# Performance work log

Measured on AMD Instinct MI355X. Metric: run time of the kernel, lower is better.

## Reference

```python
import jax, jax.numpy as jnp
import numpy as np
import math

HIDDEN = 4096
N_HEADS = 32
HEAD_DIM = HIDDEN // N_HEADS
ADAPTER_LEN = 10
BATCH = 1
SEQ = 2048
ROPE_BASE = 10000.0


def setup_inputs() -> dict:
    key = jax.random.key(0)
    ks = jax.random.split(key, 8)
    hidden_states = jax.random.normal(ks[0], (BATCH, SEQ, HIDDEN), dtype=jnp.float32)
    # additive causal mask [B,1,q,kv] with 0 on allowed, large negative on masked
    neg = jnp.finfo(jnp.float32).min
    causal = jnp.triu(jnp.full((SEQ, SEQ), neg, dtype=jnp.float32), k=1)
    attention_mask = jnp.broadcast_to(causal, (BATCH, 1, SEQ, SEQ))
    position_ids = jnp.broadcast_to(jnp.arange(SEQ, dtype=jnp.int64 if jax.config.read('jax_enable_x64') else jnp.int32)[None, :], (BATCH, SEQ))
    s = 0.02
    Wq = jax.random.normal(ks[1], (HIDDEN, HIDDEN), dtype=jnp.float32) * s
    Wk = jax.random.normal(ks[2], (HIDDEN, HIDDEN), dtype=jnp.float32) * s
    Wv = jax.random.normal(ks[3], (HIDDEN, HIDDEN), dtype=jnp.float32) * s
    Wo = jax.random.normal(ks[4], (HIDDEN, HIDDEN), dtype=jnp.float32) * s
    adapter_prefix = jax.random.normal(ks[5], (ADAPTER_LEN, HIDDEN), dtype=jnp.float32) * s
    gate = jnp.zeros((N_HEADS, 1, 1), dtype=jnp.float32) + 0.1  # nonzero so gated path is exercised
    return {"hidden_states": hidden_states, "attention_mask": attention_mask,
            "position_ids": position_ids, "Wq": Wq, "Wk": Wk, "Wv": Wv, "Wo": Wo,
            "adapter_prefix": adapter_prefix, "gate": gate}


def _rotate_half(x):
    x1, x2 = jnp.split(x, 2, axis=-1)
    return jnp.concatenate([-x2, x1], axis=-1)


def _rope_cos_sin(position_ids, head_dim, dtype):
    # inv_freq: [hd/2]
    inv_freq = 1.0 / (ROPE_BASE ** (jnp.arange(0, head_dim, 2, dtype=jnp.float32) / head_dim))
    freqs = position_ids.astype(jnp.float32)[:, :, None] * inv_freq[None, None, :]  # [B,S,hd/2]
    emb = jnp.concatenate([freqs, freqs], axis=-1)  # [B,S,hd]
    cos = jnp.cos(emb)[:, None, :, :].astype(dtype)  # [B,1,S,hd]
    sin = jnp.sin(emb)[:, None, :, :].astype(dtype)
    return cos, sin


def reference(hidden_states, attention_mask, position_ids, Wq, Wk, Wv, Wo, adapter_prefix, gate):
    B, S, H = hidden_states.shape
    nh, hd = N_HEADS, HEAD_DIM
    plen = adapter_prefix.shape[0]

    def proj(x, W):  # torch Linear: x @ W.T
        return jnp.einsum('...h,oh->...o', x, W)

    q = proj(hidden_states, Wq).reshape(B, S, nh, hd).transpose(0, 2, 1, 3)  # [B,nh,S,hd]
    k = proj(hidden_states, Wk).reshape(B, S, nh, hd).transpose(0, 2, 1, 3)
    v = proj(hidden_states, Wv).reshape(B, S, nh, hd).transpose(0, 2, 1, 3)

    cos, sin = _rope_cos_sin(position_ids, hd, q.dtype)
    q = q * cos + _rotate_half(q) * sin
    k = k * cos + _rotate_half(k) * sin

    # adapter prefix KV (bsz must be 1 per original view semantics; no RoPE applied)
    kp = proj(adapter_prefix, Wk).reshape(B, plen, nh, hd).transpose(0, 2, 1, 3)  # [B,nh,plen,hd]
    vp = proj(adapter_prefix, Wv).reshape(B, plen, nh, hd).transpose(0, 2, 1, 3)
    K = jnp.concatenate([kp, k], axis=2)  # [B,nh,plen+S,hd]
    V = jnp.concatenate([vp, v], axis=2)

    mask = jnp.concatenate([jnp.zeros((B, 1, S, plen), dtype=attention_mask.dtype), attention_mask], axis=-1)
    scores = jnp.einsum('bhqd,bhkd->bhqk', q, K) / math.sqrt(hd)
    scores = scores + mask
    scores = jnp.maximum(scores, jnp.finfo(scores.dtype).min)

    prefix_w = jax.nn.softmax(scores[..., :plen].astype(jnp.float32), axis=-1).astype(q.dtype)
    token_w = jax.nn.softmax(scores[..., plen:].astype(jnp.float32), axis=-1).astype(q.dtype)
    g = jnp.tanh(gate)[None, :, :, :]  # [1,nh,1,1]
    attn = jnp.concatenate([g * prefix_w, token_w], axis=-1)  # [B,nh,S,plen+S]

    out = jnp.einsum('bhqk,bhkd->bhqd', attn, V)  # [B,nh,S,hd]
    out = out.transpose(0, 2, 1, 3).reshape(B, S, H)
    return proj(out, Wo)
```

## Files before the change

kernel.cpp:

```cpp
#include <hip/hip_runtime.h>
#include <math.h>

#define HIDDEN 4096
#define NH 32
#define HD 128
#define PLEN 10
#define SEQQ 2048
#define QT 32
#define KT 64
#define QKVLD 12288

typedef __attribute__((ext_vector_type(8))) _Float16 f16x8;
typedef __attribute__((ext_vector_type(4))) float f32x4;

#define GLD16(g, l) __builtin_amdgcn_global_load_lds( \
        (const __attribute__((address_space(1))) void*)(g), \
        (__attribute__((address_space(3))) void*)(l), 16, 0, 0)

__global__ __launch_bounds__(256) void cvt_f16_kernel(
    const float* __restrict__ x, _Float16* __restrict__ y, int n8)
{
    int idx = blockIdx.x * 256 + threadIdx.x;
    if (idx >= n8) return;
    const float4* xp = (const float4*)x;
    float4 a = xp[idx * 2], b = xp[idx * 2 + 1];
    f16x8 o;
    o[0] = (_Float16)a.x; o[1] = (_Float16)a.y; o[2] = (_Float16)a.z; o[3] = (_Float16)a.w;
    o[4] = (_Float16)b.x; o[5] = (_Float16)b.y; o[6] = (_Float16)b.z; o[7] = (_Float16)b.w;
    *(f16x8*)(y + (size_t)idx * 8) = o;
}

__global__ __launch_bounds__(256) void cvt_pad_f16_kernel(
    const float* __restrict__ src, _Float16* __restrict__ y)
{
    int idx = blockIdx.x * 256 + threadIdx.x;
    int row = idx >> 9;
    f16x8 o;
    if (row < PLEN) {
        const float4* xp = (const float4*)src;
        float4 a = xp[idx * 2], b = xp[idx * 2 + 1];
        o[0] = (_Float16)a.x; o[1] = (_Float16)a.y; o[2] = (_Float16)a.z; o[3] = (_Float16)a.w;
        o[4] = (_Float16)b.x; o[5] = (_Float16)b.y; o[6] = (_Float16)b.z; o[7] = (_Float16)b.w;
    } else {
#pragma unroll
        for (int i = 0; i < 8; ++i) o[i] = (_Float16)0.0f;
    }
    *(f16x8*)(y + (size_t)idx * 8) = o;
}

template <typename OT>
__global__ __launch_bounds__(256) void gemm_f16_kernel(
    const _Float16* __restrict__ A, const _Float16* __restrict__ B,
    OT* __restrict__ C, int N, int K, int Mstore)
{
    __shared__ _Float16 lds[2 * 8192];

    const int tid = threadIdx.x;
    const int lane = tid & 63;
    const int wave = tid >> 6;

    const int gx = gridDim.x;
    const int nwg = gx * gridDim.y;
    const int flat = blockIdx.y * gx + blockIdx.x;
    const int cpx = nwg >> 3;
    const int sw = (flat & 7) * cpx + (flat >> 3);
    const int m0 = (sw / gx) * 128;
    const int n0 = (sw % gx) * 128;

    const _Float16* srcp = (wave < 2) ? A : B;
    const int tb = ((wave < 2) ? m0 : n0) + (wave & 1) * 64;
    const int swz = ((lane & 7) ^ ((lane >> 3) & 7)) << 3;
    const _Float16* p0 = srcp + (size_t)(tb + (lane >> 3)) * K + swz;
    _Float16* ldsw = &lds[(wave >> 1) * 8192 + (wave & 1) * 4096];

    const int lr = lane & 15;
    const int lq = lane >> 4;
    const int wm = (wave >> 1) * 64;
    const int wn = (wave & 1) * 64;

    f32x4 acc[4][4];
#pragma unroll
    for (int m = 0; m < 4; ++m)
#pragma unroll
        for (int n = 0; n < 4; ++n) acc[m][n] = (f32x4){0.f, 0.f, 0.f, 0.f};

#pragma unroll
    for (int c = 0; c < 8; ++c)
        GLD16(p0 + (size_t)c * 8 * K, ldsw + c * 512);

    const int NK = K >> 6;
    for (int ks = 0; ks < NK; ++ks) {
        __syncthreads();

#pragma unroll
        for (int kc = 0; kc < 2; ++kc) {
            f16x8 af[4], bf[4];
#pragma unroll
            for (int m = 0; m < 4; ++m) {
                int r = wm + m * 16 + lr;
                af[m] = *(const f16x8*)&lds[(r << 6) + ((((kc << 2) + lq) ^ (lr & 7)) << 3)];
            }
#pragma unroll
            for (int n = 0; n < 4; ++n) {
                int r = wn + n * 16 + lr;
                bf[n] = *(const f16x8*)&lds[8192 + (r << 6) + ((((kc << 2) + lq) ^ (lr & 7)) << 3)];
            }
#pragma unroll
            for (int m = 0; m < 4; ++m)
#pragma unroll
                for (int n = 0; n < 4; ++n)
                    acc[m][n] = __builtin_amdgcn_mfma_f32_16x16x32_f16(af[m], bf[n], acc[m][n], 0, 0, 0);
        }

        __syncthreads();
        if (ks + 1 < NK) {
            const int k0 = (ks + 1) << 6;
#pragma unroll
            for (int c = 0; c < 8; ++c)
                GLD16(p0 + (size_t)c * 8 * K + k0, ldsw + c * 512);
        }
    }

#pragma unroll
    for (int m = 0; m < 4; ++m) {
        const int row = m0 + wm + m * 16 + lq * 4;
#pragma unroll
        for (int n = 0; n < 4; ++n) {
            const int col = n0 + wn + n * 16 + lr;
#pragma unroll
            for (int j = 0; j < 4; ++j)
                if (row + j < Mstore)
                    C[(size_t)(row + j) * N + col] = (OT)acc[m][n][j];
        }
    }
}

__global__ void rope_table_kernel(const int* __restrict__ pos,
                                  float* __restrict__ cosT, float* __restrict__ sinT)
{
    int s = blockIdx.x;
    int j = threadIdx.x;
    float p = (float)pos[s];
    float expnt = (2.0f * (float)j) * (1.0f / 128.0f);
    float inv_freq = powf(10000.0f, -expnt);
    float f = p * inv_freq;
    cosT[s * 64 + j] = cosf(f);
    sinT[s * 64 + j] = sinf(f);
}

__global__ void rope_f16ip_kernel(_Float16* __restrict__ qkv,
                                  const float* __restrict__ cosT, const float* __restrict__ sinT)
{
    int idx = blockIdx.x * 256 + threadIdx.x;
    int s = idx >> 11;
    int rem = idx & 2047;
    int h = rem >> 6;
    int d = rem & 63;
    float c = cosT[s * 64 + d], sn = sinT[s * 64 + d];
    size_t base = (size_t)s * QKVLD + h * HD + d;
    float a = (float)qkv[base], b = (float)qkv[base + 64];
    qkv[base]      = (_Float16)(a * c - b * sn);
    qkv[base + 64] = (_Float16)(b * c + a * sn);
    size_t kb = base + HIDDEN;
    a = (float)qkv[kb]; b = (float)qkv[kb + 64];
    qkv[kb]      = (_Float16)(a * c - b * sn);
    qkv[kb + 64] = (_Float16)(b * c + a * sn);
}

__global__ __launch_bounds__(256) void vtrans_f16_kernel(
    const _Float16* __restrict__ v, _Float16* __restrict__ vt)
{
    __shared__ _Float16 Vs[64][136];
    const int h = blockIdx.y;
    const int s0 = blockIdx.x * 64;
    const int tid = threadIdx.x;
#pragma unroll
    for (int i = 0; i < 4; ++i) {
        int flat = tid + 256 * i;
        int r = flat >> 4;
        int c8 = (flat & 15) * 8;
        *(f16x8*)&Vs[r][c8] = *(const f16x8*)(v + (size_t)(s0 + r) * QKVLD + h * HD + c8);
    }
    __syncthreads();
#pragma unroll
    for (int pass = 0; pass < 4; ++pass) {
        int d = pass * 32 + (tid >> 3);
        int sb = (tid & 7) * 8;
        f16x8 o;
#pragma unroll
        for (int e = 0; e < 8; ++e) o[e] = Vs[sb + e][d];
        *(f16x8*)(vt + ((size_t)h * HD + d) * SEQQ + s0 + sb) = o;
    }
}

__global__ __launch_bounds__(256) void attn_f16_kernel(
    const _Float16* __restrict__ Qf, const _Float16* __restrict__ Kf,
    const _Float16* __restrict__ Vtf,
    const float* __restrict__ kp, const float* __restrict__ vp,
    const float* __restrict__ gate, _Float16* __restrict__ out)
{
    __shared__ _Float16 KVs[64 * 128];
    __shared__ float Ps[4][16][68];
    __shared__ float Pp[4][16][12];

    const int h = blockIdx.x;
    const int q0 = blockIdx.y * 64;
    const int tid = threadIdx.x;
    const int wave = tid >> 6;
    const int lane = tid & 63;
    const int lr = lane & 15;
    const int lq = lane >> 4;
    const float scale = 0.088388347648318447f;
    const float scale2 = 0.088388347648318447f * 1.4426950408889634f;

    const int qrow = q0 + wave * 16 + lr;
    f16x8 qh[4];
#pragma unroll
    for (int c = 0; c < 4; ++c)
        qh[c] = *(const f16x8*)(Qf + (size_t)qrow * QKVLD + h * HD + c * 32 + lq * 8);

    f32x4 accO[8];
#pragma unroll
    for (int n = 0; n < 8; ++n) accO[n] = (f32x4){0.f, 0.f, 0.f, 0.f};
    float m_run[4] = {-INFINITY, -INFINITY, -INFINITY, -INFINITY};
    float l_run[4] = {0.f, 0.f, 0.f, 0.f};

    const int ntiles = blockIdx.y + 1;
    for (int t = 0; t < ntiles; ++t) {
        const int j0 = t * 64;
        __syncthreads();

        {
            const int rl = lane >> 4;
            const int ch = lane & 15;
#pragma unroll
            for (int ii = 0; ii < 4; ++ii) {
                int r = wave * 16 + ii * 4 + rl;
                int chs = ch ^ (r & 7);
                const _Float16* g = Kf + (size_t)(j0 + r) * QKVLD + h * HD + chs * 8;
                GLD16(g, &KVs[(wave * 16 + ii * 4) * 128]);
            }
        }
        __syncthreads();

        f32x4 sacc[4];
#pragma unroll
        for (int n = 0; n < 4; ++n) sacc[n] = (f32x4){0.f, 0.f, 0.f, 0.f};
#pragma unroll
        for (int c = 0; c < 4; ++c) {
#pragma unroll
            for (int n = 0; n < 4; ++n) {
                int row = n * 16 + lr;
                int chs = (4 * c + lq) ^ (lr & 7);
                f16x8 kf8 = *(const f16x8*)&KVs[row * 128 + chs * 8];
                sacc[n] = __builtin_amdgcn_mfma_f32_16x16x32_f16(qh[c], kf8, sacc[n], 0, 0, 0);
            }
        }

#pragma unroll
        for (int j = 0; j < 4; ++j) {
            const int grow = q0 + wave * 16 + lq * 4 + j;
#pragma unroll
            for (int n = 0; n < 4; ++n) {
                int gcol = j0 + n * 16 + lr;
                float val = sacc[n][j] * scale2;
                sacc[n][j] = (gcol > grow) ? -INFINITY : val;
            }
            float mx = fmaxf(fmaxf(sacc[0][j], sacc[1][j]), fmaxf(sacc[2][j], sacc[3][j]));
            mx = fmaxf(mx, __shfl_xor(mx, 1));
            mx = fmaxf(mx, __shfl_xor(mx, 2));
            mx = fmaxf(mx, __shfl_xor(mx, 4));
            mx = fmaxf(mx, __shfl_xor(mx, 8));
            float mn = fmaxf(m_run[j], mx);
            float corr = exp2f(m_run[j] - mn);
            m_run[j] = mn;
            float ls = 0.f;
#pragma unroll
            for (int n = 0; n < 4; ++n) {
                float p = exp2f(sacc[n][j] - mn);
                Ps[wave][lq * 4 + j][n * 16 + lr] = p;
                ls += p;
            }
            ls += __shfl_xor(ls, 1);
            ls += __shfl_xor(ls, 2);
            ls += __shfl_xor(ls, 4);
            ls += __shfl_xor(ls, 8);
            l_run[j] = l_run[j] * corr + ls;
#pragma unroll
            for (int n = 0; n < 8; ++n) accO[n][j] *= corr;
        }

        __syncthreads();

        {
            const int dl = lane >> 3;
            const int vch = lane & 7;
#pragma unroll
            for (int ii = 0; ii < 4; ++ii) {
                int d = wave * 32 + ii * 8 + dl;
                int chs = vch ^ (d & 7);
                const _Float16* g = Vtf + ((size_t)h * HD + d) * SEQQ + j0 + chs * 8;
                GLD16(g, &KVs[(wave * 32 + ii * 8) * 64]);
            }
        }
        __syncthreads();

#pragma unroll
        for (int jc = 0; jc < 2; ++jc) {
            float pv[8];
            *(float4*)&pv[0] = *(const float4*)&Ps[wave][lr][jc * 32 + lq * 8];
            *(float4*)&pv[4] = *(const float4*)&Ps[wave][lr][jc * 32 + lq * 8 + 4];
            f16x8 pa;
#pragma unroll
            for (int e = 0; e < 8; ++e) pa[e] = (_Float16)pv[e];
#pragma unroll
            for (int n = 0; n < 8; ++n) {
                int row = n * 16 + lr;
                int chv = (jc * 4 + lq) ^ (lr & 7);
                f16x8 vf = *(const f16x8*)&KVs[row * 64 + chv * 8];
                accO[n] = __builtin_amdgcn_mfma_f32_16x16x32_f16(pa, vf, accO[n], 0, 0, 0);
            }
        }
    }

#pragma unroll
    for (int j = 0; j < 4; ++j) {
        float inv_l = 1.0f / l_run[j];
#pragma unroll
        for (int n = 0; n < 8; ++n) accO[n][j] *= inv_l;
    }

    {
        float g = tanhf(gate[h]);
        float sp[PLEN];
        float mp = -INFINITY;
#pragma unroll
        for (int i = 0; i < PLEN; ++i) {
            const float* kpr = kp + (size_t)i * QKVLD + h * HD;
            float s = 0.f;
#pragma unroll
            for (int c = 0; c < 4; ++c)
#pragma unroll
                for (int e = 0; e < 8; ++e)
                    s = fmaf((float)qh[c][e], kpr[c * 32 + lq * 8 + e], s);
            s += __shfl_xor(s, 16);
            s += __shfl_xor(s, 32);
            sp[i] = s * scale;
            mp = fmaxf(mp, sp[i]);
        }
        float ssum = 0.f;
#pragma unroll
        for (int i = 0; i < PLEN; ++i) { sp[i] = expf(sp[i] - mp); ssum += sp[i]; }
        float gs = g / ssum;
        if (lq == 0) {
#pragma unroll
            for (int i = 0; i < PLEN; ++i) Pp[wave][lr][i] = sp[i] * gs;
        }
#pragma unroll
        for (int i = 0; i < PLEN; ++i) {
            float vv[8];
#pragma unroll
            for (int n = 0; n < 8; ++n)
                vv[n] = vp[(size_t)i * QKVLD + h * HD + n * 16 + lr];
#pragma unroll
            for (int j = 0; j < 4; ++j) {
                float w = Pp[wave][lq * 4 + j][i];
#pragma unroll
                for (int n = 0; n < 8; ++n) accO[n][j] = fmaf(w, vv[n], accO[n][j]);
            }
        }
    }

#pragma unroll
    for (int n = 0; n < 8; ++n)
#pragma unroll
        for (int j = 0; j < 4; ++j)
            out[(size_t)(q0 + wave * 16 + lq * 4 + j) * HIDDEN + h * HD + n * 16 + lr] =
                (_Float16)accO[n][j];
}

__global__ __launch_bounds__(256) void gemm_nt_kernel(
    const float* __restrict__ A, const float* __restrict__ B, float* __restrict__ C,
    int M, int N, int K)
{
    __shared__ float As[8][132];
    __shared__ float Bs[8][132];
    const int tid = threadIdx.x;
    const int tx = tid & 15, ty = tid >> 4;
    const int m0 = blockIdx.y * 128, n0 = blockIdx.x * 128;
    const int lr = tid >> 1;
    const int lk = (tid & 1) * 4;
    const bool aval = (m0 + lr) < M;
    const float* Ap = A + (size_t)(m0 + lr) * K + lk;
    const float* Bp = B + (size_t)(n0 + lr) * K + lk;

    float acc[8][8];
#pragma unroll
    for (int i = 0; i < 8; ++i)
#pragma unroll
        for (int j = 0; j < 8; ++j) acc[i][j] = 0.0f;

    for (int k0 = 0; k0 < K; k0 += 8) {
        float4 a4 = make_float4(0.f, 0.f, 0.f, 0.f);
        if (aval) a4 = *(const float4*)(Ap + k0);
        float4 b4 = *(const float4*)(Bp + k0);
        __syncthreads();
        As[lk + 0][lr] = a4.x; As[lk + 1][lr] = a4.y; As[lk + 2][lr] = a4.z; As[lk + 3][lr] = a4.w;
        Bs[lk + 0][lr] = b4.x; Bs[lk + 1][lr] = b4.y; Bs[lk + 2][lr] = b4.z; Bs[lk + 3][lr] = b4.w;
        __syncthreads();
#pragma unroll
        for (int kk = 0; kk < 8; ++kk) {
            float4 a0 = *(const float4*)&As[kk][ty * 8];
            float4 a1 = *(const float4*)&As[kk][ty * 8 + 4];
            float4 b0 = *(const float4*)&Bs[kk][tx * 8];
            float4 b1 = *(const float4*)&Bs[kk][tx * 8 + 4];
            float a[8] = {a0.x, a0.y, a0.z, a0.w, a1.x, a1.y, a1.z, a1.w};
            float b[8] = {b0.x, b0.y, b0.z, b0.w, b1.x, b1.y, b1.z, b1.w};
#pragma unroll
            for (int i = 0; i < 8; ++i)
#pragma unroll
                for (int j = 0; j < 8; ++j)
                    acc[i][j] = fmaf(a[i], b[j], acc[i][j]);
        }
    }
#pragma unroll
    for (int i = 0; i < 8; ++i) {
        int row = m0 + ty * 8 + i;
        if (row < M) {
            float* Cp = C + (size_t)row * N + n0 + tx * 8;
            *(float4*)Cp       = make_float4(acc[i][0], acc[i][1], acc[i][2], acc[i][3]);
            *(float4*)(Cp + 4) = make_float4(acc[i][4], acc[i][5], acc[i][6], acc[i][7]);
        }
    }
}

__global__ void rope_apply_kernel(float* __restrict__ q, float* __restrict__ k,
                                  const float* __restrict__ cosT, const float* __restrict__ sinT)
{
    int idx = blockIdx.x * 256 + threadIdx.x;
    int s = idx >> 11;
    int rem = idx & 2047;
    int h = rem >> 6;
    int d = rem & 63;
    float c = cosT[s * 64 + d], sn = sinT[s * 64 + d];
    size_t base = (size_t)s * HIDDEN + h * HD + d;
    float a = q[base], b = q[base + 64];
    q[base]      = a * c - b * sn;
    q[base + 64] = b * c + a * sn;
    a = k[base]; b = k[base + 64];
    k[base]      = a * c - b * sn;
    k[base + 64] = b * c + a * sn;
}

__global__ __launch_bounds__(256) void attn_kernel(
    const float* __restrict__ q, const float* __restrict__ k, const float* __restrict__ v,
    const float* __restrict__ kp, const float* __restrict__ vp,
    const float* __restrict__ gate, float* __restrict__ out)
{
    __shared__ float Qt[128][36];
    __shared__ float KV[128 * 68];
    __shared__ float Psh[QT][68];

    const int h = blockIdx.y;
    const int r0 = blockIdx.x * QT;
    const int tid = threadIdx.x;
    const int orow = tid >> 3;
    const int oc4 = (tid & 7) * 4;
    const int sy = tid >> 4;
    const int sx = tid & 15;
    const float scale = 0.088388347648318447f;

#pragma unroll
    for (int i = 0; i < 4; ++i) {
        int flat = tid + 256 * i;
        int r = flat >> 5;
        int d = (flat & 31) << 2;
        float4 t = *(const float4*)(q + (size_t)(r0 + r) * HIDDEN + h * HD + d);
        Qt[d + 0][r] = t.x; Qt[d + 1][r] = t.y; Qt[d + 2][r] = t.z; Qt[d + 3][r] = t.w;
    }

    float acc[4][4];
#pragma unroll
    for (int u = 0; u < 4; ++u)
#pragma unroll
        for (int i = 0; i < 4; ++i) acc[u][i] = 0.0f;
    float m_run = -INFINITY, l_run = 0.0f;

    const int jb_max = (r0 + QT - 1) >> 6;
    for (int jb = 0; jb <= jb_max; ++jb) {
        const int j0 = jb * KT;
        __syncthreads();
#pragma unroll
        for (int i = 0; i < 8; ++i) {
            int flat = tid + 256 * i;
            int r = flat >> 5;
            int d = (flat & 31) << 2;
            float4 t = *(const float4*)(k + (size_t)(j0 + r) * HIDDEN + h * HD + d);
            KV[(d + 0) * 68 + r] = t.x; KV[(d + 1) * 68 + r] = t.y;
            KV[(d + 2) * 68 + r] = t.z; KV[(d + 3) * 68 + r] = t.w;
        }
        __syncthreads();
        float s8[2][4] = {{0.f, 0.f, 0.f, 0.f}, {0.f, 0.f, 0.f, 0.f}};
        for (int d = 0; d < 128; ++d) {
            float2 qv = *(const float2*)&Qt[d][sy * 2];
            float4 kv4 = *(const float4*)&KV[d * 68 + sx * 4];
            s8[0][0] = fmaf(qv.x, kv4.x, s8[0][0]);
            s8[0][1] = fmaf(qv.x, kv4.y, s8[0][1]);
            s8[0][2] = fmaf(qv.x, kv4.z, s8[0][2]);
            s8[0][3] = fmaf(qv.x, kv4.w, s8[0][3]);
            s8[1][0] = fmaf(qv.y, kv4.x, s8[1][0]);
            s8[1][1] = fmaf(qv.y, kv4.y, s8[1][1]);
            s8[1][2] = fmaf(qv.y, kv4.z, s8[1][2]);
            s8[1][3] = fmaf(qv.y, kv4.w, s8[1][3]);
        }
#pragma unroll
        for (int i = 0; i < 2; ++i) {
            int gr = r0 + sy * 2 + i;
#pragma unroll
            for (int jj = 0; jj < 4; ++jj) {
                int gj = j0 + sx * 4 + jj;
                float val = s8[i][jj] * scale;
                Psh[sy * 2 + i][sx * 4 + jj] = (gj > gr) ? -INFINITY : val;
            }
        }
        __syncthreads();
        {
            const int c0 = (tid & 7) * 8;
            float sv[8];
            float mx = -INFINITY;
#pragma unroll
            for (int i = 0; i < 8; ++i) { sv[i] = Psh[orow][c0 + i]; mx = fmaxf(mx, sv[i]); }
            mx = fmaxf(mx, __shfl_xor(mx, 1));
            mx = fmaxf(mx, __shfl_xor(mx, 2));
            mx = fmaxf(mx, __shfl_xor(mx, 4));
            float m_new = fmaxf(m_run, mx);
            float corr = expf(m_run - m_new);
            float lsum = 0.f;
#pragma unroll
            for (int i = 0; i < 8; ++i) {
                float p = expf(sv[i] - m_new);
                Psh[orow][c0 + i] = p;
                lsum += p;
            }
            lsum += __shfl_xor(lsum, 1);
            lsum += __shfl_xor(lsum, 2);
            lsum += __shfl_xor(lsum, 4);
            l_run = l_run * corr + lsum;
            m_run = m_new;
#pragma unroll
            for (int u = 0; u < 4; ++u)
#pragma unroll
                for (int i = 0; i < 4; ++i) acc[u][i] *= corr;
        }
        __syncthreads();
#pragma unroll
        for (int i = 0; i < 8; ++i) {
            int flat = tid + 256 * i;
            int r = flat >> 5;
            int d = (flat & 31) << 2;
            float4 t = *(const float4*)(v + (size_t)(j0 + r) * HIDDEN + h * HD + d);
            *(float4*)&KV[r * 136 + d] = t;
        }
        __syncthreads();
        for (int j = 0; j < KT; ++j) {
            float p = Psh[orow][j];
#pragma unroll
            for (int u = 0; u < 4; ++u) {
                float4 vv = *(const float4*)&KV[j * 136 + oc4 + u * 32];
                acc[u][0] = fmaf(p, vv.x, acc[u][0]);
                acc[u][1] = fmaf(p, vv.y, acc[u][1]);
                acc[u][2] = fmaf(p, vv.z, acc[u][2]);
                acc[u][3] = fmaf(p, vv.w, acc[u][3]);
            }
        }
    }

    float inv_l = 1.0f / l_run;
#pragma unroll
    for (int u = 0; u < 4; ++u)
#pragma unroll
        for (int i = 0; i < 4; ++i) acc[u][i] *= inv_l;

    {
        float g = tanhf(gate[h]);
        float sp[PLEN];
        float mp = -INFINITY;
#pragma unroll
        for (int i = 0; i < PLEN; ++i) {
            const float* kpr = kp + (size_t)i * HIDDEN + h * HD;
            float s = 0.f;
            for (int d = 0; d < 128; ++d) s = fmaf(Qt[d][orow], kpr[d], s);
            sp[i] = s * scale;
            mp = fmaxf(mp, sp[i]);
        }
        float ssum = 0.f;
#pragma unroll
        for (int i = 0; i < PLEN; ++i) { sp[i] = expf(sp[i] - mp); ssum += sp[i]; }
        float gs = g / ssum;
#pragma unroll
        for (int i = 0; i < PLEN; ++i) {
            float w = sp[i] * gs;
            const float* vpr = vp + (size_t)i * HIDDEN + h * HD;
#pragma unroll
            for (int u = 0; u < 4; ++u) {
                float4 vv = *(const float4*)(vpr + oc4 + u * 32);
                acc[u][0] = fmaf(w, vv.x, acc[u][0]);
                acc[u][1] = fmaf(w, vv.y, acc[u][1]);
                acc[u][2] = fmaf(w, vv.z, acc[u][2]);
                acc[u][3] = fmaf(w, vv.w, acc[u][3]);
            }
        }
    }

    float* op = out + (size_t)(r0 + orow) * HIDDEN + h * HD;
#pragma unroll
    for (int u = 0; u < 4; ++u)
        *(float4*)(op + oc4 + u * 32) = make_float4(acc[u][0], acc[u][1], acc[u][2], acc[u][3]);
}

extern "C" void kernel_launch(void* const* d_in, const int* in_sizes, int n_in,
                              void* d_out, int out_size, void* d_ws, size_t ws_size,
                              hipStream_t stream)
{
    (void)in_sizes; (void)n_in; (void)out_size;
    const float* hidden  = (const float*)d_in[0];
    const int*   pos     = (const int*)d_in[2];
    const float* Wq      = (const float*)d_in[3];
    const float* Wk      = (const float*)d_in[4];
    const float* Wv      = (const float*)d_in[5];
    const float* Wo      = (const float*)d_in[6];
    const float* adapter = (const float*)d_in[7];
    const float* gate    = (const float*)d_in[8];
    float* out = (float*)d_out;

    const size_t SH = (size_t)SEQQ * HIDDEN;
    const size_t WN = (size_t)HIDDEN * HIDDEN;
    const size_t PN = (size_t)128 * HIDDEN;

    float* cosT = (float*)d_ws;
    float* sinT = cosT + (size_t)SEQQ * 64;
    float* AP   = sinT + (size_t)SEQQ * 64;
    _Float16* Hf    = (_Float16*)(AP + (size_t)128 * QKVLD);
    _Float16* Wqkvf = Hf + SH;
    _Float16* Pf    = Wqkvf + 3 * WN;
    _Float16* QKVf  = Pf + PN;
    _Float16* Vtf   = QKVf + 3 * SH;
    const size_t need = (size_t)((char*)(Vtf + SH) - (char*)d_ws);
    const bool use_f16 = (ws_size >= need);

    _Float16* Of  = Hf;
    _Float16* Wof = Wqkvf;

    rope_table_kernel<<<SEQQ, 64, 0, stream>>>(pos, cosT, sinT);

    dim3 blk(256);
    const int nH8 = (int)(SH / 8);
    const int nW8 = (int)(WN / 8);

    if (use_f16) {
        cvt_f16_kernel<<<nH8 / 256, blk, 0, stream>>>(hidden, Hf, nH8);
        cvt_f16_kernel<<<nW8 / 256, blk, 0, stream>>>(Wq, Wqkvf, nW8);
        cvt_f16_kernel<<<nW8 / 256, blk, 0, stream>>>(Wk, Wqkvf + WN, nW8);
        cvt_f16_kernel<<<nW8 / 256, blk, 0, stream>>>(Wv, Wqkvf + 2 * WN, nW8);
        cvt_pad_f16_kernel<<<(int)(PN / 8 / 256), blk, 0, stream>>>(adapter, Pf);

        gemm_f16_kernel<_Float16><<<dim3(QKVLD / 128, SEQQ / 128), blk, 0, stream>>>(
            Hf, Wqkvf, QKVf, QKVLD, HIDDEN, SEQQ);
        gemm_f16_kernel<float><<<dim3(QKVLD / 128, 1), blk, 0, stream>>>(
            Pf, Wqkvf, AP, QKVLD, HIDDEN, PLEN);

        rope_f16ip_kernel<<<(SEQQ * 2048) / 256, blk, 0, stream>>>(QKVf, cosT, sinT);
        vtrans_f16_kernel<<<dim3(SEQQ / 64, NH), blk, 0, stream>>>(QKVf + 2 * HIDDEN, Vtf);

        attn_f16_kernel<<<dim3(NH, SEQQ / 64), blk, 0, stream>>>(
            QKVf, QKVf + HIDDEN, Vtf, AP + HIDDEN, AP + 2 * HIDDEN, gate, Of);

        cvt_f16_kernel<<<nW8 / 256, blk, 0, stream>>>(Wo, Wof, nW8);
        gemm_f16_kernel<float><<<dim3(HIDDEN / 128, SEQQ / 128), blk, 0, stream>>>(
            Of, Wof, out, HIDDEN, HIDDEN, SEQQ);
    } else {
        float* ws = (float*)d_ws;
        float* qb   = ws;
        float* kb   = ws + SH;
        float* vb   = ws + 2 * SH;
        float* kpb  = ws + 3 * SH;
        float* vpb  = kpb + (size_t)PLEN * HIDDEN;
        float* cT   = vpb + (size_t)PLEN * HIDDEN;
        float* sT   = cT + (size_t)SEQQ * 64;
        rope_table_kernel<<<SEQQ, 64, 0, stream>>>(pos, cT, sT);
        dim3 gbig(HIDDEN / 128, SEQQ / 128);
        dim3 gsm(HIDDEN / 128, 1);
        gemm_nt_kernel<<<gbig, blk, 0, stream>>>(hidden, Wq, qb, SEQQ, HIDDEN, HIDDEN);
        gemm_nt_kernel<<<gbig, blk, 0, stream>>>(hidden, Wk, kb, SEQQ, HIDDEN, HIDDEN);
        gemm_nt_kernel<<<gbig, blk, 0, stream>>>(hidden, Wv, vb, SEQQ, HIDDEN, HIDDEN);
        gemm_nt_kernel<<<gsm, blk, 0, stream>>>(adapter, Wk, kpb, PLEN, HIDDEN, HIDDEN);
        gemm_nt_kernel<<<gsm, blk, 0, stream>>>(adapter, Wv, vpb, PLEN, HIDDEN, HIDDEN);
        rope_apply_kernel<<<(SEQQ * 2048) / 256, 256, 0, stream>>>(qb, kb, cT, sT);
        attn_kernel<<<dim3(SEQQ / QT, NH), blk, 0, stream>>>(qb, kb, vb, kpb, vpb, gate, qb);
        gemm_nt_kernel<<<gbig, blk, 0, stream>>>(qb, Wo, out, SEQQ, HIDDEN, HIDDEN);
    }
}
```

Measured before the change: 643.8 us.

## Add double-buffered 256x128 GEMM for QKV/output projections and store P as f16

Introduces a new 512-thread GEMM kernel with 256x128 tiles and double-buffered LDS. It issues async global-to-LDS loads for the next K slice while MFMAs run on the current one and raises wave priority around the MFMA block. Both large projections (fused QKV and output) now use it. Separately, the attention kernel writes softmax probabilities to LDS as f16 instead of f32, which halves that LDS traffic and removes the per-iteration conversion. The trade-off is heavier LDS use per block (96KB) and higher register pressure, which may lower occupancy.

```diff
diff --git a/kernel.cpp b/kernel.cpp
--- a/kernel.cpp
+++ b/kernel.cpp
@@ -46,6 +46,103 @@
         for (int i = 0; i < 8; ++i) o[i] = (_Float16)0.0f;
     }
     *(f16x8*)(y + (size_t)idx * 8) = o;
+}
+
+template <typename OT>
+__global__ __launch_bounds__(512) void gemm_f16_db_kernel(
+    const _Float16* __restrict__ A, const _Float16* __restrict__ B,
+    OT* __restrict__ C, int N, int K, int Mstore)
+{
+    __shared__ _Float16 ldsA[2][256 * 64];
+    __shared__ _Float16 ldsB[2][128 * 64];
+
+    const int tid = threadIdx.x;
+    const int lane = tid & 63;
+    const int wave = tid >> 6;
+
+    const int gx = gridDim.x;
+    const int nwg = gx * gridDim.y;
+    const int flat = blockIdx.y * gx + blockIdx.x;
+    const int cpx = nwg >> 3;
+    const int sw = (flat & 7) * cpx + (flat >> 3);
+    const int m0 = (sw / gx) * 256;
+    const int n0 = (sw % gx) * 128;
+
+    const int wm = wave >> 2;
+    const int wn = wave & 3;
+    const int lr = lane & 15;
+    const int lq = lane >> 4;
+
+    const int srow = lane >> 3;
+    const int sswz = ((lane & 7) ^ srow) << 3;
+    const _Float16* gA = A + (size_t)(m0 + wave * 32 + srow) * K + sswz;
+    const _Float16* gB = B + (size_t)(n0 + wave * 16 + srow) * K + sswz;
+
+    f32x4 acc[8][2];
+#pragma unroll
+    for (int m = 0; m < 8; ++m)
+#pragma unroll
+        for (int n = 0; n < 2; ++n) acc[m][n] = (f32x4){0.f, 0.f, 0.f, 0.f};
+
+    {
+        _Float16* dA = &ldsA[0][(wave * 32) * 64];
+        GLD16(gA, dA);
+        GLD16(gA + 8 * (size_t)K, dA + 512);
+        GLD16(gA + 16 * (size_t)K, dA + 1024);
+        GLD16(gA + 24 * (size_t)K, dA + 1536);
+        _Float16* dB = &ldsB[0][(wave * 16) * 64];
+        GLD16(gB, dB);
+        GLD16(gB + 8 * (size_t)K, dB + 512);
+    }
+    __syncthreads();
+
+    const int NK = K >> 6;
+    for (int t = 0; t < NK; ++t) {
+        const int cur = t & 1;
+        if (t + 1 < NK) {
+            const size_t ko = (size_t)(t + 1) << 6;
+            _Float16* dA = &ldsA[cur ^ 1][(wave * 32) * 64];
+            GLD16(gA + ko, dA);
+            GLD16(gA + ko + 8 * (size_t)K, dA + 512);
+            GLD16(gA + ko + 16 * (size_t)K, dA + 1024);
+            GLD16(gA + ko + 24 * (size_t)K, dA + 1536);
+            _Float16* dB = &ldsB[cur ^ 1][(wave * 16) * 64];
+            GLD16(gB + ko, dB);
+            GLD16(gB + ko + 8 * (size_t)K, dB + 512);
+        }
+#pragma unroll
+        for (int kc = 0; kc < 2; ++kc) {
+            const int slot = (((kc << 2) + lq) ^ (lr & 7)) << 3;
+            f16x8 bfr[2], afr[8];
+#pragma unroll
+            for (int n = 0; n < 2; ++n)
+                bfr[n] = *(const f16x8*)&ldsB[cur][(wn * 32 + n * 16 + lr) * 64 + slot];
+#pragma unroll
+            for (int m = 0; m < 8; ++m)
+                afr[m] = *(const f16x8*)&ldsA[cur][(wm * 128 + m * 16 + lr) * 64 + slot];
+            __builtin_amdgcn_s_setprio(1);
+#pragma unroll
+            for (int m = 0; m < 8; ++m)
+#pragma unroll
+                for (int n = 0; n < 2; ++n)
+                    acc[m][n] = __builtin_amdgcn_mfma_f32_16x16x32_f16(afr[m], bfr[n], acc[m][n], 0, 0, 0);
+            __builtin_amdgcn_s_setprio(0);
+        }
+        __syncthreads();
+    }
+
+#pragma unroll
+    for (int m = 0; m < 8; ++m) {
+        const int row = m0 + wm * 128 + m * 16 + lq * 4;
+#pragma unroll
+        for (int n = 0; n < 2; ++n) {
+            const int col = n0 + wn * 32 + n * 16 + lr;
+#pragma unroll
+            for (int j = 0; j < 4; ++j)
+                if (row + j < Mstore)
+                    C[(size_t)(row + j) * N + col] = (OT)acc[m][n][j];
+        }
+    }
 }
 
 template <typename OT>
@@ -200,7 +297,7 @@
     const float* __restrict__ gate, _Float16* __restrict__ out)
 {
     __shared__ _Float16 KVs[64 * 128];
-    __shared__ float Ps[4][16][68];
+    __shared__ _Float16 Psh[4][16][72];
     __shared__ float Pp[4][16][12];
 
     const int h = blockIdx.x;
@@ -278,7 +375,7 @@
 #pragma unroll
             for (int n = 0; n < 4; ++n) {
                 float p = exp2f(sacc[n][j] - mn);
-                Ps[wave][lq * 4 + j][n * 16 + lr] = p;
+                Psh[wave][lq * 4 + j][n * 16 + lr] = (_Float16)p;
                 ls += p;
             }
             ls += __shfl_xor(ls, 1);
@@ -307,12 +404,7 @@
 
 #pragma unroll
         for (int jc = 0; jc < 2; ++jc) {
-            float pv[8];
-            *(float4*)&pv[0] = *(const float4*)&Ps[wave][lr][jc * 32 + lq * 8];
-            *(float4*)&pv[4] = *(const float4*)&Ps[wave][lr][jc * 32 + lq * 8 + 4];
-            f16x8 pa;
-#pragma unroll
-            for (int e = 0; e < 8; ++e) pa[e] = (_Float16)pv[e];
+            f16x8 pa = *(const f16x8*)&Psh[wave][lr][jc * 32 + lq * 8];
 #pragma unroll
             for (int n = 0; n < 8; ++n) {
                 int row = n * 16 + lr;
@@ -459,7 +551,7 @@
 {
     __shared__ float Qt[128][36];
     __shared__ float KV[128 * 68];
-    __shared__ float Psh[QT][68];
+    __shared__ float Psh2[QT][68];
 
     const int h = blockIdx.y;
     const int r0 = blockIdx.x * QT;
@@ -520,7 +612,7 @@
             for (int jj = 0; jj < 4; ++jj) {
                 int gj = j0 + sx * 4 + jj;
                 float val = s8[i][jj] * scale;
-                Psh[sy * 2 + i][sx * 4 + jj] = (gj > gr) ? -INFINITY : val;
+                Psh2[sy * 2 + i][sx * 4 + jj] = (gj > gr) ? -INFINITY : val;
             }
         }
         __syncthreads();
@@ -529,7 +621,7 @@
             float sv[8];
             float mx = -INFINITY;
 #pragma unroll
-            for (int i = 0; i < 8; ++i) { sv[i] = Psh[orow][c0 + i]; mx = fmaxf(mx, sv[i]); }
+            for (int i = 0; i < 8; ++i) { sv[i] = Psh2[orow][c0 + i]; mx = fmaxf(mx, sv[i]); }
             mx = fmaxf(mx, __shfl_xor(mx, 1));
             mx = fmaxf(mx, __shfl_xor(mx, 2));
             mx = fmaxf(mx, __shfl_xor(mx, 4));
@@ -539,7 +631,7 @@
 #pragma unroll
             for (int i = 0; i < 8; ++i) {
                 float p = expf(sv[i] - m_new);
-                Psh[orow][c0 + i] = p;
+                Psh2[orow][c0 + i] = p;
                 lsum += p;
             }
             lsum += __shfl_xor(lsum, 1);
@@ -563,7 +655,7 @@
         }
         __syncthreads();
         for (int j = 0; j < KT; ++j) {
-            float p = Psh[orow][j];
+            float p = Psh2[orow][j];
 #pragma unroll
             for (int u = 0; u < 4; ++u) {
                 float4 vv = *(const float4*)&KV[j * 136 + oc4 + u * 32];
@@ -664,7 +756,7 @@
         cvt_f16_kernel<<<nW8 / 256, blk, 0, stream>>>(Wv, Wqkvf + 2 * WN, nW8);
         cvt_pad_f16_kernel<<<(int)(PN / 8 / 256), blk, 0, stream>>>(adapter, Pf);
 
-        gemm_f16_kernel<_Float16><<<dim3(QKVLD / 128, SEQQ / 128), blk, 0, stream>>>(
+        gemm_f16_db_kernel<_Float16><<<dim3(QKVLD / 128, SEQQ / 256), dim3(512), 0, stream>>>(
             Hf, Wqkvf, QKVf, QKVLD, HIDDEN, SEQQ);
         gemm_f16_kernel<float><<<dim3(QKVLD / 128, 1), blk, 0, stream>>>(
             Pf, Wqkvf, AP, QKVLD, HIDDEN, PLEN);
@@ -676,7 +768,7 @@
             QKVf, QKVf + HIDDEN, Vtf, AP + HIDDEN, AP + 2 * HIDDEN, gate, Of);
 
         cvt_f16_kernel<<<nW8 / 256, blk, 0, stream>>>(Wo, Wof, nW8);
-        gemm_f16_kernel<float><<<dim3(HIDDEN / 128, SEQQ / 128), blk, 0, stream>>>(
+        gemm_f16_db_kernel<float><<<dim3(HIDDEN / 128, SEQQ / 256), dim3(512), 0, stream>>>(
             Of, Wof, out, HIDDEN, HIDDEN, SEQQ);
     } else {
         float* ws = (float*)d_ws;
```

Result: slower. 673.5 us (+4.6%).

## Balance causal attention by pairing query tiles, store P as fp16, add MFMA priority

Applied to the files above, without the earlier changes.

The attention kernel now launches half as many blocks per head, and each block processes query tile bb and its mirror 31-bb. Every block therefore does the same amount of causal work, removing the tail from unequal tile lengths. The softmax probabilities are written to shared memory as fp16, so the fp32 reload and per-element conversion before the PV MFMA go away. s_setprio is raised around MFMA sections in both the GEMM and attention kernels, and the GEMM tile swizzle is reordered to walk along M first. Halving the block count reduces the number of concurrent blocks, which may lower occupancy.

```diff
diff --git a/kernel.cpp b/kernel.cpp
--- a/kernel.cpp
+++ b/kernel.cpp
@@ -60,12 +60,13 @@
     const int wave = tid >> 6;
 
     const int gx = gridDim.x;
-    const int nwg = gx * gridDim.y;
+    const int gy = gridDim.y;
+    const int nwg = gx * gy;
     const int flat = blockIdx.y * gx + blockIdx.x;
     const int cpx = nwg >> 3;
     const int sw = (flat & 7) * cpx + (flat >> 3);
-    const int m0 = (sw / gx) * 128;
-    const int n0 = (sw % gx) * 128;
+    const int m0 = (sw % gy) * 128;
+    const int n0 = (sw / gy) * 128;
 
     const _Float16* srcp = (wave < 2) ? A : B;
     const int tb = ((wave < 2) ? m0 : n0) + (wave & 1) * 64;
@@ -105,11 +106,13 @@
                 int r = wn + n * 16 + lr;
                 bf[n] = *(const f16x8*)&lds[8192 + (r << 6) + ((((kc << 2) + lq) ^ (lr & 7)) << 3)];
             }
+            __builtin_amdgcn_s_setprio(1);
 #pragma unroll
             for (int m = 0; m < 4; ++m)
 #pragma unroll
                 for (int n = 0; n < 4; ++n)
                     acc[m][n] = __builtin_amdgcn_mfma_f32_16x16x32_f16(af[m], bf[n], acc[m][n], 0, 0, 0);
+            __builtin_amdgcn_s_setprio(0);
         }
 
         __syncthreads();
@@ -200,11 +203,11 @@
     const float* __restrict__ gate, _Float16* __restrict__ out)
 {
     __shared__ _Float16 KVs[64 * 128];
-    __shared__ float Ps[4][16][68];
+    __shared__ _Float16 Psh[4][16][72];
     __shared__ float Pp[4][16][12];
 
     const int h = blockIdx.x;
-    const int q0 = blockIdx.y * 64;
+    const int bb = blockIdx.y;
     const int tid = threadIdx.x;
     const int wave = tid >> 6;
     const int lane = tid & 63;
@@ -213,170 +216,176 @@
     const float scale = 0.088388347648318447f;
     const float scale2 = 0.088388347648318447f * 1.4426950408889634f;
 
-    const int qrow = q0 + wave * 16 + lr;
-    f16x8 qh[4];
-#pragma unroll
-    for (int c = 0; c < 4; ++c)
-        qh[c] = *(const f16x8*)(Qf + (size_t)qrow * QKVLD + h * HD + c * 32 + lq * 8);
-
-    f32x4 accO[8];
-#pragma unroll
-    for (int n = 0; n < 8; ++n) accO[n] = (f32x4){0.f, 0.f, 0.f, 0.f};
-    float m_run[4] = {-INFINITY, -INFINITY, -INFINITY, -INFINITY};
-    float l_run[4] = {0.f, 0.f, 0.f, 0.f};
-
-    const int ntiles = blockIdx.y + 1;
-    for (int t = 0; t < ntiles; ++t) {
-        const int j0 = t * 64;
-        __syncthreads();
+    for (int pp = 0; pp < 2; ++pp) {
+        const int qt = pp ? (31 - bb) : bb;
+        const int q0 = qt * 64;
+
+        const int qrow = q0 + wave * 16 + lr;
+        f16x8 qh[4];
+#pragma unroll
+        for (int c = 0; c < 4; ++c)
+            qh[c] = *(const f16x8*)(Qf + (size_t)qrow * QKVLD + h * HD + c * 32 + lq * 8);
+
+        f32x4 accO[8];
+#pragma unroll
+        for (int n = 0; n < 8; ++n) accO[n] = (f32x4){0.f, 0.f, 0.f, 0.f};
+        float m_run[4] = {-INFINITY, -INFINITY, -INFINITY, -INFINITY};
+        float l_run[4] = {0.f, 0.f, 0.f, 0.f};
+
+        const int ntiles = qt + 1;
+        for (int t = 0; t < ntiles; ++t) {
+            const int j0 = t * 64;
+            __syncthreads();
+
+            {
+                const int rl = lane >> 4;
+                const int ch = lane & 15;
+#pragma unroll
+                for (int ii = 0; ii < 4; ++ii) {
+                    int r = wave * 16 + ii * 4 + rl;
+                    int chs = ch ^ (r & 7);
+                    const _Float16* g = Kf + (size_t)(j0 + r) * QKVLD + h * HD + chs * 8;
+                    GLD16(g, &KVs[(wave * 16 + ii * 4) * 128]);
+                }
+            }
+            __syncthreads();
+
+            f32x4 sacc[4];
+#pragma unroll
+            for (int n = 0; n < 4; ++n) sacc[n] = (f32x4){0.f, 0.f, 0.f, 0.f};
+            __builtin_amdgcn_s_setprio(1);
+#pragma unroll
+            for (int c = 0; c < 4; ++c) {
+#pragma unroll
+                for (int n = 0; n < 4; ++n) {
+                    int row = n * 16 + lr;
+                    int chs = (4 * c + lq) ^ (lr & 7);
+                    f16x8 kf8 = *(const f16x8*)&KVs[row * 128 + chs * 8];
+                    sacc[n] = __builtin_amdgcn_mfma_f32_16x16x32_f16(qh[c], kf8, sacc[n], 0, 0, 0);
+                }
+            }
+            __builtin_amdgcn_s_setprio(0);
+
+#pragma unroll
+            for (int j = 0; j < 4; ++j) {
+                const int grow = q0 + wave * 16 + lq * 4 + j;
+#pragma unroll
+                for (int n = 0; n < 4; ++n) {
+                    int gcol = j0 + n * 16 + lr;
+                    float val = sacc[n][j] * scale2;
+                    sacc[n][j] = (gcol > grow) ? -INFINITY : val;
+                }
+                float mx = fmaxf(fmaxf(sacc[0][j], sacc[1][j]), fmaxf(sacc[2][j], sacc[3][j]));
+                mx = fmaxf(mx, __shfl_xor(mx, 1));
+                mx = fmaxf(mx, __shfl_xor(mx, 2));
+                mx = fmaxf(mx, __shfl_xor(mx, 4));
+                mx = fmaxf(mx, __shfl_xor(mx, 8));
+                float mn = fmaxf(m_run[j], mx);
+                float corr = exp2f(m_run[j] - mn);
+                m_run[j] = mn;
+                float ls = 0.f;
+#pragma unroll
+                for (int n = 0; n < 4; ++n) {
+                    float p = exp2f(sacc[n][j] - mn);
+                    Psh[wave][lq * 4 + j][n * 16 + lr] = (_Float16)p;
+                    ls += p;
+                }
+                ls += __shfl_xor(ls, 1);
+                ls += __shfl_xor(ls, 2);
+                ls += __shfl_xor(ls, 4);
+                ls += __shfl_xor(ls, 8);
+                l_run[j] = l_run[j] * corr + ls;
+#pragma unroll
+                for (int n = 0; n < 8; ++n) accO[n][j] *= corr;
+            }
+
+            __syncthreads();
+
+            {
+                const int dl = lane >> 3;
+                const int vch = lane & 7;
+#pragma unroll
+                for (int ii = 0; ii < 4; ++ii) {
+                    int d = wave * 32 + ii * 8 + dl;
+                    int chs = vch ^ (d & 7);
+                    const _Float16* g = Vtf + ((size_t)h * HD + d) * SEQQ + j0 + chs * 8;
+                    GLD16(g, &KVs[(wave * 32 + ii * 8) * 64]);
+                }
+            }
+            __syncthreads();
+
+            __builtin_amdgcn_s_setprio(1);
+#pragma unroll
+            for (int jc = 0; jc < 2; ++jc) {
+                f16x8 pa = *(const f16x8*)&Psh[wave][lr][jc * 32 + lq * 8];
+#pragma unroll
+                for (int n = 0; n < 8; ++n) {
+                    int row = n * 16 + lr;
+                    int chv = (jc * 4 + lq) ^ (lr & 7);
+                    f16x8 vf = *(const f16x8*)&KVs[row * 64 + chv * 8];
+                    accO[n] = __builtin_amdgcn_mfma_f32_16x16x32_f16(pa, vf, accO[n], 0, 0, 0);
+                }
+            }
+            __builtin_amdgcn_s_setprio(0);
+        }
+
+#pragma unroll
+        for (int j = 0; j < 4; ++j) {
+            float inv_l = 1.0f / l_run[j];
+#pragma unroll
+            for (int n = 0; n < 8; ++n) accO[n][j] *= inv_l;
+        }
 
         {
-            const int rl = lane >> 4;
-            const int ch = lane & 15;
-#pragma unroll
-            for (int ii = 0; ii < 4; ++ii) {
-                int r = wave * 16 + ii * 4 + rl;
-                int chs = ch ^ (r & 7);
-                const _Float16* g = Kf + (size_t)(j0 + r) * QKVLD + h * HD + chs * 8;
-                GLD16(g, &KVs[(wave * 16 + ii * 4) * 128]);
-            }
-        }
-        __syncthreads();
-
-        f32x4 sacc[4];
-#pragma unroll
-        for (int n = 0; n < 4; ++n) sacc[n] = (f32x4){0.f, 0.f, 0.f, 0.f};
-#pragma unroll
-        for (int c = 0; c < 4; ++c) {
-#pragma unroll
-            for (int n = 0; n < 4; ++n) {
-                int row = n * 16 + lr;
-                int chs = (4 * c + lq) ^ (lr & 7);
-                f16x8 kf8 = *(const f16x8*)&KVs[row * 128 + chs * 8];
-                sacc[n] = __builtin_amdgcn_mfma_f32_16x16x32_f16(qh[c], kf8, sacc[n], 0, 0, 0);
-            }
-        }
-
-#pragma unroll
-        for (int j = 0; j < 4; ++j) {
-            const int grow = q0 + wave * 16 + lq * 4 + j;
-#pragma unroll
-            for (int n = 0; n < 4; ++n) {
-                int gcol = j0 + n * 16 + lr;
-                float val = sacc[n][j] * scale2;
-                sacc[n][j] = (gcol > grow) ? -INFINITY : val;
-            }
-            float mx = fmaxf(fmaxf(sacc[0][j], sacc[1][j]), fmaxf(sacc[2][j], sacc[3][j]));
-            mx = fmaxf(mx, __shfl_xor(mx, 1));
-            mx = fmaxf(mx, __shfl_xor(mx, 2));
-            mx = fmaxf(mx, __shfl_xor(mx, 4));
-            mx = fmaxf(mx, __shfl_xor(mx, 8));
-            float mn = fmaxf(m_run[j], mx);
-            float corr = exp2f(m_run[j] - mn);
-            m_run[j] = mn;
-            float ls = 0.f;
-#pragma unroll
-            for (int n = 0; n < 4; ++n) {
-                float p = exp2f(sacc[n][j] - mn);
-                Ps[wave][lq * 4 + j][n * 16 + lr] = p;
-                ls += p;
-            }
-            ls += __shfl_xor(ls, 1);
-            ls += __shfl_xor(ls, 2);
-            ls += __shfl_xor(ls, 4);
-            ls += __shfl_xor(ls, 8);
-            l_run[j] = l_run[j] * corr + ls;
-#pragma unroll
-            for (int n = 0; n < 8; ++n) accO[n][j] *= corr;
-        }
-
-        __syncthreads();
-
-        {
-            const int dl = lane >> 3;
-            const int vch = lane & 7;
-#pragma unroll
-            for (int ii = 0; ii < 4; ++ii) {
-                int d = wave * 32 + ii * 8 + dl;
-                int chs = vch ^ (d & 7);
-                const _Float16* g = Vtf + ((size_t)h * HD + d) * SEQQ + j0 + chs * 8;
-                GLD16(g, &KVs[(wave * 32 + ii * 8) * 64]);
-            }
-        }
-        __syncthreads();
-
-#pragma unroll
-        for (int jc = 0; jc < 2; ++jc) {
-            float pv[8];
-            *(float4*)&pv[0] = *(const float4*)&Ps[wave][lr][jc * 32 + lq * 8];
-            *(float4*)&pv[4] = *(const float4*)&Ps[wave][lr][jc * 32 + lq * 8 + 4];
-            f16x8 pa;
-#pragma unroll
-            for (int e = 0; e < 8; ++e) pa[e] = (_Float16)pv[e];
-#pragma unroll
-            for (int n = 0; n < 8; ++n) {
-                int row = n * 16 + lr;
-                int chv = (jc * 4 + lq) ^ (lr & 7);
-                f16x8 vf = *(const f16x8*)&KVs[row * 64 + chv * 8];
-                accO[n] = __builtin_amdgcn_mfma_f32_16x16x32_f16(pa, vf, accO[n], 0, 0, 0);
-            }
-        }
-    }
-
-#pragma unroll
-    for (int j = 0; j < 4; ++j) {
-        float inv_l = 1.0f / l_run[j];
-#pragma unroll
-        for (int n = 0; n < 8; ++n) accO[n][j] *= inv_l;
-    }
-
-    {
-        float g = tanhf(gate[h]);
-        float sp[PLEN];
-        float mp = -INFINITY;
-#pragma unroll
-        for (int i = 0; i < PLEN; ++i) {
-            const float* kpr = kp + (size_t)i * QKVLD + h * HD;
-            float s = 0.f;
-#pragma unroll
-            for (int c = 0; c < 4; ++c)
-#pragma unroll
-                for (int e = 0; e < 8; ++e)
-                    s = fmaf((float)qh[c][e], kpr[c * 32 + lq * 8 + e], s);
-            s += __shfl_xor(s, 16);
-            s += __shfl_xor(s, 32);
-            sp[i] = s * scale;
-            mp = fmaxf(mp, sp[i]);
-        }
-        float ssum = 0.f;
-#pragma unroll
-        for (int i = 0; i < PLEN; ++i) { sp[i] = expf(sp[i] - mp); ssum += sp[i]; }
-        float gs = g / ssum;
-        if (lq == 0) {
-#pragma unroll
-            for (int i = 0; i < PLEN; ++i) Pp[wave][lr][i] = sp[i] * gs;
-        }
-#pragma unroll
-        for (int i = 0; i < PLEN; ++i) {
-            float vv[8];
-#pragma unroll
-            for (int n = 0; n < 8; ++n)
-                vv[n] = vp[(size_t)i * QKVLD + h * HD + n * 16 + lr];
-#pragma unroll
-            for (int j = 0; j < 4; ++j) {
-                float w = Pp[wave][lq * 4 + j][i];
-#pragma unroll
-                for (int n = 0; n < 8; ++n) accO[n][j] = fmaf(w, vv[n], accO[n][j]);
-            }
-        }
-    }
-
-#pragma unroll
-    for (int n = 0; n < 8; ++n)
-#pragma unroll
-        for (int j = 0; j < 4; ++j)
-            out[(size_t)(q0 + wave * 16 + lq * 4 + j) * HIDDEN + h * HD + n * 16 + lr] =
-                (_Float16)accO[n][j];
+            float g = tanhf(gate[h]);
+            float sp[PLEN];
+            float mp = -INFINITY;
+#pragma unroll
+            for (int i = 0; i < PLEN; ++i) {
+                const float* kpr = kp + (size_t)i * QKVLD + h * HD;
+                float s = 0.f;
+#pragma unroll
+                for (int c = 0; c < 4; ++c)
+#pragma unroll
+                    for (int e = 0; e < 8; ++e)
+                        s = fmaf((float)qh[c][e], kpr[c * 32 + lq * 8 + e], s);
+                s += __shfl_xor(s, 16);
+                s += __shfl_xor(s, 32);
+                sp[i] = s * scale;
+                mp = fmaxf(mp, sp[i]);
+            }
+            float ssum = 0.f;
+#pragma unroll
+            for (int i = 0; i < PLEN; ++i) { sp[i] = expf(sp[i] - mp); ssum += sp[i]; }
+            float gs = g / ssum;
+            if (lq == 0) {
+#pragma unroll
+                for (int i = 0; i < PLEN; ++i) Pp[wave][lr][i] = sp[i] * gs;
+            }
+#pragma unroll
+            for (int i = 0; i < PLEN; ++i) {
+                float vv[8];
+#pragma unroll
+                for (int n = 0; n < 8; ++n)
+                    vv[n] = vp[(size_t)i * QKVLD + h * HD + n * 16 + lr];
+#pragma unroll
+                for (int j = 0; j < 4; ++j) {
+                    float w = Pp[wave][lq * 4 + j][i];
+#pragma unroll
+                    for (int n = 0; n < 8; ++n) accO[n][j] = fmaf(w, vv[n], accO[n][j]);
+                }
+            }
+        }
+
+#pragma unroll
+        for (int n = 0; n < 8; ++n)
+#pragma unroll
+            for (int j = 0; j < 4; ++j)
+                out[(size_t)(q0 + wave * 16 + lq * 4 + j) * HIDDEN + h * HD + n * 16 + lr] =
+                    (_Float16)accO[n][j];
+
+        __syncthreads();
+    }
 }
 
 __global__ __launch_bounds__(256) void gemm_nt_kernel(
@@ -459,7 +468,7 @@
 {
     __shared__ float Qt[128][36];
     __shared__ float KV[128 * 68];
-    __shared__ float Psh[QT][68];
+    __shared__ float Psh2[QT][68];
 
     const int h = blockIdx.y;
     const int r0 = blockIdx.x * QT;
@@ -520,7 +529,7 @@
             for (int jj = 0; jj < 4; ++jj) {
                 int gj = j0 + sx * 4 + jj;
                 float val = s8[i][jj] * scale;
-                Psh[sy * 2 + i][sx * 4 + jj] = (gj > gr) ? -INFINITY : val;
+                Psh2[sy * 2 + i][sx * 4 + jj] = (gj > gr) ? -INFINITY : val;
             }
         }
         __syncthreads();
@@ -529,7 +538,7 @@
             float sv[8];
             float mx = -INFINITY;
 #pragma unroll
-            for (int i = 0; i < 8; ++i) { sv[i] = Psh[orow][c0 + i]; mx = fmaxf(mx, sv[i]); }
+            for (int i = 0; i < 8; ++i) { sv[i] = Psh2[orow][c0 + i]; mx = fmaxf(mx, sv[i]); }
             mx = fmaxf(mx, __shfl_xor(mx, 1));
             mx = fmaxf(mx, __shfl_xor(mx, 2));
             mx = fmaxf(mx, __shfl_xor(mx, 4));
@@ -539,7 +548,7 @@
 #pragma unroll
             for (int i = 0; i < 8; ++i) {
                 float p = expf(sv[i] - m_new);
-                Psh[orow][c0 + i] = p;
+                Psh2[orow][c0 + i] = p;
                 lsum += p;
             }
             lsum += __shfl_xor(lsum, 1);
@@ -563,7 +572,7 @@
         }
         __syncthreads();
         for (int j = 0; j < KT; ++j) {
-            float p = Psh[orow][j];
+            float p = Psh2[orow][j];
 #pragma unroll
             for (int u = 0; u < 4; ++u) {
                 float4 vv = *(const float4*)&KV[j * 136 + oc4 + u * 32];
@@ -672,7 +681,7 @@
         rope_f16ip_kernel<<<(SEQQ * 2048) / 256, blk, 0, stream>>>(QKVf, cosT, sinT);
         vtrans_f16_kernel<<<dim3(SEQQ / 64, NH), blk, 0, stream>>>(QKVf + 2 * HIDDEN, Vtf);
 
-        attn_f16_kernel<<<dim3(NH, SEQQ / 64), blk, 0, stream>>>(
+        attn_f16_kernel<<<dim3(NH, 16), blk, 0, stream>>>(
             QKVf, QKVf + HIDDEN, Vtf, AP + HIDDEN, AP + 2 * HIDDEN, gate, Of);
 
         cvt_f16_kernel<<<nW8 / 256, blk, 0, stream>>>(Wo, Wof, nW8);
```

After: 724.9 us. +12.6%, slower.
